# Optimization experiments

Hardware: AMD Instinct MI355X
Metric: run time of the kernel (lower is better)

## Reference

```python
import jax, jax.numpy as jnp
import numpy as np

E = 32      # num_embodiments
A = 64      # action_dim
H = 1024    # hidden_size
B = 64
T = 64


def setup_inputs() -> dict:
    key = jax.random.key(0)
    ks = jax.random.split(key, 9)
    return {
        "actions": jax.random.normal(ks[0], (B, T, A), dtype=jnp.float32),
        "W1_W": 0.02 * jax.random.normal(ks[1], (E, A, H), dtype=jnp.float32),
        "W1_b": jnp.zeros((E, H), dtype=jnp.float32),
        "W2_W": 0.02 * jax.random.normal(ks[2], (E, 2 * H, H), dtype=jnp.float32),
        "W2_b": jnp.zeros((E, H), dtype=jnp.float32),
        "W3_W": 0.02 * jax.random.normal(ks[3], (E, H, H), dtype=jnp.float32),
        "W3_b": jnp.zeros((E, H), dtype=jnp.float32),
        "timesteps": jax.random.randint(ks[4], (B,), 0, 1000, dtype=jnp.int32),
        "cat_ids": jax.random.randint(ks[5], (B,), 0, E, dtype=jnp.int32),
    }


def _cat_linear(x, W, b, cat_ids):
    # x: (B,T,in), W: (E,in,out), b: (E,out)
    Wg = W[cat_ids]               # (B,in,out) gathered per-batch weights
    bg = b[cat_ids]               # (B,out)
    return jnp.einsum('bti,bio->bto', x, Wg) + bg[:, None, :]


def _sinusoidal_pe(t, dim):
    # t: (B,T) float -> (B,T,dim)
    half = dim // 2
    exponent = -jnp.arange(half, dtype=jnp.float32) * (jnp.log(jnp.float32(10000.0)) / half)
    freqs = t[..., None] * jnp.exp(exponent)
    return jnp.concatenate([jnp.sin(freqs), jnp.cos(freqs)], axis=-1)


def reference(actions, W1_W, W1_b, W2_W, W2_b, W3_W, W3_b, timesteps, cat_ids):
    b, t, _ = actions.shape
    ts = jnp.broadcast_to(timesteps.astype(jnp.float32)[:, None], (b, t))  # (B,T)
    a_emb = _cat_linear(actions, W1_W, W1_b, cat_ids)                      # (B,T,H)
    tau_emb = _sinusoidal_pe(ts, H).astype(a_emb.dtype)                    # (B,T,H)
    x = jnp.concatenate([a_emb, tau_emb], axis=-1)                         # (B,T,2H)
    h = _cat_linear(x, W2_W, W2_b, cat_ids)
    x = h * jax.nn.sigmoid(h)                                              # swish
    return _cat_linear(x, W3_W, W3_b, cat_ids)                             # (B,T,H)
```

## Files before the change

### kernel.cpp

```cpp
#include <hip/hip_runtime.h>
#include <hip/hip_bf16.h>

#define NB 64
#define NT 64
#define NA 64
#define NH 1024
#define NE 32
#define K2DIM 2048

typedef unsigned short bf16_t;
typedef __attribute__((ext_vector_type(8))) short bf16x8;
typedef __attribute__((ext_vector_type(4))) short s16x4;
typedef __attribute__((ext_vector_type(4))) float f32x4;

__device__ __forceinline__ bf16_t f32_to_bf16(float f) {
    unsigned int u = __float_as_uint(f);
    u = (u + 0x7FFFu + ((u >> 16) & 1u)) >> 16;
    return (bf16_t)u;
}
__device__ __forceinline__ unsigned cvt2(float x, float y) {
    unsigned short a = __builtin_bit_cast(unsigned short, __float2bfloat16(x));
    unsigned short b = __builtin_bit_cast(unsigned short, __float2bfloat16(y));
    return (unsigned)a | ((unsigned)b << 16);
}

__global__ void make_groups(const int* __restrict__ cat_ids,
                            int* __restrict__ groups)
{
    __shared__ int keys[NB], order[NB], catv[NB];
    __shared__ int gcat[NB], gnb[NB], gb[NB][4];
    __shared__ int sng;

    const int tid = threadIdx.x;
    int c = cat_ids[tid];
    catv[tid] = c;
    keys[tid] = c * 64 + tid;
    __syncthreads();

    int mykey = keys[tid];
    int rank = 0;
    for (int j = 0; j < NB; ++j) rank += (keys[j] < mykey) ? 1 : 0;
    order[rank] = tid;
    __syncthreads();

    if (tid == 0) {
        int ng = 0, prev = -1, cnt = 4;
        for (int i = 0; i < NB; ++i) {
            int b  = order[i];
            int cb = catv[b];
            if (cb != prev || cnt == 4) {
                gcat[ng] = cb; gnb[ng] = 0; cnt = 0; prev = cb; ++ng;
            }
            gb[ng - 1][cnt] = b;
            ++cnt; gnb[ng - 1] = cnt;
        }
        sng = ng;
    }
    __syncthreads();

    int ng = sng;
    int base = tid * 8;
    if (tid < ng) {
        int nbv = gnb[tid];
        groups[base + 0] = gcat[tid];
        groups[base + 1] = nbv;
        #pragma unroll
        for (int s = 0; s < 4; ++s)
            groups[base + 2 + s] = gb[tid][s < nbv ? s : 0];
        groups[base + 6] = 0; groups[base + 7] = 0;
    } else {
        #pragma unroll
        for (int s = 0; s < 8; ++s) groups[base + s] = 0;
    }
}

__global__ __launch_bounds__(256) void k1_embed(
    const float* __restrict__ actions, const float* __restrict__ W1,
    const float* __restrict__ b1, const int* __restrict__ timesteps,
    const int* __restrict__ cat_ids, bf16_t* __restrict__ x)
{
    __shared__ float act[NT][NA];
    __shared__ float pe[64];

    const int b   = blockIdx.x;
    const int c0  = blockIdx.y * 64;
    const int tid = threadIdx.x;
    const int cat = cat_ids[b];
    const float ts = (float)timesteps[b];

    const float* ab = actions + b * (NT * NA);
    #pragma unroll
    for (int p = 0; p < 16; ++p) {
        int idx = tid + p * 256;
        act[idx >> 6][idx & 63] = ab[idx];
    }
    if (tid < 64) {
        const float kfreq = logf(10000.0f) / 512.0f;
        int c = c0 + tid;
        float v;
        if (c < 512) v = sinf(ts * expf(-(float)c * kfreq));
        else         v = cosf(ts * expf(-(float)(c - 512) * kfreq));
        pe[tid] = v;
    }
    __syncthreads();

    const int cc = tid & 63;
    const int c  = c0 + cc;
    const int t0 = tid >> 6;

    float acc[16];
    const float bias = b1[cat * NH + c];
    #pragma unroll
    for (int i = 0; i < 16; ++i) acc[i] = bias;

    const float* Wp = W1 + (size_t)cat * (NA * NH) + c;
    #pragma unroll 8
    for (int k = 0; k < NA; ++k) {
        float w = Wp[(size_t)k * NH];
        #pragma unroll
        for (int i = 0; i < 16; ++i)
            acc[i] = fmaf(act[t0 + 4 * i][k], w, acc[i]);
    }

    bf16_t* xb = x + (size_t)b * (NT * K2DIM);
    const bf16_t pv = f32_to_bf16(pe[cc]);
    #pragma unroll
    for (int i = 0; i < 16; ++i) {
        int t = t0 + 4 * i;
        xb[(size_t)t * K2DIM + c]      = f32_to_bf16(acc[i]);
        xb[(size_t)t * K2DIM + NH + c] = pv;
    }
}

template<int KDIM, bool SWISH, typename OutT>
__global__ __launch_bounds__(512) void gemm_grouped(
    const bf16_t* __restrict__ xin, const float* __restrict__ W,
    const float* __restrict__ bias, const int* __restrict__ groups,
    OutT* __restrict__ out)
{
    __shared__ __align__(128) char xs[4 * 8192];
    __shared__ __align__(128) char wsm[16384];

    const int* grp = groups + blockIdx.x * 8;
    const int nb = grp[1];
    if (nb == 0) return;
    const int cat = grp[0];
    int bslot[4];
    #pragma unroll
    for (int s = 0; s < 4; ++s) bslot[s] = grp[2 + s];

    const int n0   = blockIdx.y * 128;
    const int tid  = threadIdx.x;
    const int lane = tid & 63;
    const int wv   = tid >> 6;
    const int l15  = lane & 15;
    const int l4   = lane >> 4;
    const int msl  = wv & 3;
    const int pw   = (wv >> 2) * 4;
    const int ncol0 = n0 + (wv >> 2) * 64;

    constexpr int NK = KDIM / 64;

    const int xt  = tid >> 3;
    const int xk8 = tid & 7;
    const int xoff = ((xt * 128 + xk8 * 16) ^ ((xt & 7) << 4));
    const bf16_t* xsrc[4];
    #pragma unroll
    for (int p = 0; p < 4; ++p)
        xsrc[p] = xin + ((size_t)bslot[p] * NT + xt) * KDIM + xk8 * 8;
    const int wk  = tid >> 4;
    const int oct = tid & 15;
    const float* Wt0 = W + (size_t)cat * KDIM * NH + n0
                         + (size_t)wk * NH + oct * 8;
    int woff[2];
    #pragma unroll
    for (int p = 0; p < 2; ++p) {
        int kk = wk + 32 * p;
        woff[p] = ((kk >> 2) * 8 + (oct >> 1)) * 128 + (kk & 3) * 32 + (oct & 1) * 16;
    }

    f32x4 acc[4][4];
    #pragma unroll
    for (int nf = 0; nf < 4; ++nf) {
        float bv = bias[(size_t)cat * NH + ncol0 + nf * 16 + l15];
        #pragma unroll
        for (int mf = 0; mf < 4; ++mf)
            acc[mf][nf] = (f32x4){bv, bv, bv, bv};
    }

    const unsigned wbase = (unsigned)(unsigned long long)&wsm[0];
    const unsigned laneB = wbase + (unsigned)(l4 * 2048 + l15 * 8);
    const int aslot = msl * 8192;

    uint4  xr[4];
    float4 wr[4];

    auto LOAD = [&](int kc) {
        #pragma unroll
        for (int p = 0; p < 4; ++p)
            xr[p] = *(const uint4*)(xsrc[p] + (size_t)kc * 64);
        #pragma unroll
        for (int p = 0; p < 2; ++p) {
            const float* s = Wt0 + (size_t)(kc * 64 + 32 * p) * NH;
            wr[2 * p]     = *(const float4*)(s);
            wr[2 * p + 1] = *(const float4*)(s + 4);
        }
    };
    auto WRITE = [&]() {
        #pragma unroll
        for (int p = 0; p < 4; ++p)
            *(uint4*)(xs + xoff + p * 8192) = xr[p];
        #pragma unroll
        for (int p = 0; p < 2; ++p) {
            uint4 pk;
            pk.x = cvt2(wr[2 * p].x,     wr[2 * p].y);
            pk.y = cvt2(wr[2 * p].z,     wr[2 * p].w);
            pk.z = cvt2(wr[2 * p + 1].x, wr[2 * p + 1].y);
            pk.w = cvt2(wr[2 * p + 1].z, wr[2 * p + 1].w);
            *(uint4*)(wsm + woff[p]) = pk;
        }
    };

    LOAD(0);
    for (int kc = 0; kc < NK; ++kc) {
        __syncthreads();
        WRITE();
        __syncthreads();
        if (kc + 1 < NK) LOAD(kc + 1);

        #pragma unroll
        for (int ks = 0; ks < 2; ++ks) {
            bf16x8 af[4], bfr[4];
            #pragma unroll
            for (int mf = 0; mf < 4; ++mf) {
                int row = mf * 16 + l15;
                int off = aslot + ((row * 128 + ks * 64 + l4 * 16) ^ ((row & 7) << 4));
                af[mf] = *(const bf16x8*)(xs + off);
            }
            #pragma unroll
            for (int nf = 0; nf < 4; ++nf) {
                unsigned a = laneB + (unsigned)(ks * 8192 + (pw + nf) * 128);
                s16x4 lo, hi;
                asm volatile("ds_read_b64_tr_b16 %0, %1" : "=v"(lo) : "v"(a));
                asm volatile("ds_read_b64_tr_b16 %0, %1 offset:1024" : "=v"(hi) : "v"(a));
                bfr[nf] = __builtin_shufflevector(lo, hi, 0, 1, 2, 3, 4, 5, 6, 7);
            }
            asm volatile("s_waitcnt lgkmcnt(0)" ::: "memory");
            __builtin_amdgcn_sched_barrier(0);
            #pragma unroll
            for (int mf = 0; mf < 4; ++mf)
                #pragma unroll
                for (int nf = 0; nf < 4; ++nf)
                    acc[mf][nf] = __builtin_amdgcn_mfma_f32_16x16x32_bf16(
                        af[mf], bfr[nf], acc[mf][nf], 0, 0, 0);
        }
    }

    const int bout = bslot[msl];
    #pragma unroll
    for (int mf = 0; mf < 4; ++mf) {
        #pragma unroll
        for (int nf = 0; nf < 4; ++nf) {
            int col = ncol0 + nf * 16 + l15;
            #pragma unroll
            for (int r = 0; r < 4; ++r) {
                int trow = mf * 16 + l4 * 4 + r;
                float h = acc[mf][nf][r];
                if (SWISH) h = h / (1.0f + __expf(-h));
                if constexpr (sizeof(OutT) == 2) {
                    out[((size_t)bout * NT + trow) * NH + col] = (OutT)f32_to_bf16(h);
                } else {
                    out[((size_t)bout * NT + trow) * NH + col] = h;
                }
            }
        }
    }
}

extern "C" void kernel_launch(void* const* d_in, const int* in_sizes, int n_in,
                              void* d_out, int out_size, void* d_ws, size_t ws_size,
                              hipStream_t stream) {
    const float* actions   = (const float*)d_in[0];
    const float* W1        = (const float*)d_in[1];
    const float* b1        = (const float*)d_in[2];
    const float* W2        = (const float*)d_in[3];
    const float* b2        = (const float*)d_in[4];
    const float* W3        = (const float*)d_in[5];
    const float* b3        = (const float*)d_in[6];
    const int*   timesteps = (const int*)d_in[7];
    const int*   cat_ids   = (const int*)d_in[8];
    float* out = (float*)d_out;

    bf16_t* x = (bf16_t*)d_ws;
    bf16_t* y = x + (size_t)NB * NT * K2DIM;
    int* groups = (int*)(y + (size_t)NB * NT * NH);

    make_groups<<<1, 64, 0, stream>>>(cat_ids, groups);
    k1_embed<<<dim3(NB, NH / 64), 256, 0, stream>>>(actions, W1, b1, timesteps, cat_ids, x);
    gemm_grouped<K2DIM, true,  bf16_t><<<dim3(64, NH / 128), 512, 0, stream>>>(x, W2, b2, groups, y);
    gemm_grouped<NH,    false, float ><<<dim3(64, NH / 128), 512, 0, stream>>>(y, W3, b3, groups, out);
}
```

Baseline: 193.9 us.

## Shrink grouped GEMM tiles to two batches and double-buffer LDS

Batches now share an embodiment group in pairs rather than fours, and each block computes a 128x64 output tile with a 32-wide K chunk instead of 256x128 with 64-wide chunks. LDS is double-buffered, so there is one barrier per chunk and the next chunk's global load overlaps the MFMAs. The grid grows to 16x64 blocks with launch bounds allowing 4 blocks per CU, which raises occupancy and parallelism. The cost is more reloads of each weight tile, since fewer batches share it, and only four MFMAs per barrier, so the arithmetic per sync is small.

```diff
diff --git a/kernel.cpp b/kernel.cpp
--- a/kernel.cpp
+++ b/kernel.cpp
@@ -28,7 +28,7 @@
                             int* __restrict__ groups)
 {
     __shared__ int keys[NB], order[NB], catv[NB];
-    __shared__ int gcat[NB], gnb[NB], gb[NB][4];
+    __shared__ int gcat[NB], gnb[NB], gb[NB][2];
     __shared__ int sng;
 
     const int tid = threadIdx.x;
@@ -44,11 +44,11 @@
     __syncthreads();
 
     if (tid == 0) {
-        int ng = 0, prev = -1, cnt = 4;
+        int ng = 0, prev = -1, cnt = 2;
         for (int i = 0; i < NB; ++i) {
             int b  = order[i];
             int cb = catv[b];
-            if (cb != prev || cnt == 4) {
+            if (cb != prev || cnt == 2) {
                 gcat[ng] = cb; gnb[ng] = 0; cnt = 0; prev = cb; ++ng;
             }
             gb[ng - 1][cnt] = b;
@@ -64,9 +64,9 @@
         int nbv = gnb[tid];
         groups[base + 0] = gcat[tid];
         groups[base + 1] = nbv;
-        #pragma unroll
-        for (int s = 0; s < 4; ++s)
-            groups[base + 2 + s] = gb[tid][s < nbv ? s : 0];
+        groups[base + 2] = gb[tid][0];
+        groups[base + 3] = (nbv > 1) ? gb[tid][1] : gb[tid][0];
+        groups[base + 4] = 0; groups[base + 5] = 0;
         groups[base + 6] = 0; groups[base + 7] = 0;
     } else {
         #pragma unroll
@@ -133,139 +133,107 @@
 }
 
 template<int KDIM, bool SWISH, typename OutT>
-__global__ __launch_bounds__(512) void gemm_grouped(
+__global__ __launch_bounds__(512, 4) void gemm_g2(
     const bf16_t* __restrict__ xin, const float* __restrict__ W,
     const float* __restrict__ bias, const int* __restrict__ groups,
     OutT* __restrict__ out)
 {
-    __shared__ __align__(128) char xs[4 * 8192];
-    __shared__ __align__(128) char wsm[16384];
-
-    const int* grp = groups + blockIdx.x * 8;
+    __shared__ __align__(128) char lds[2][12288];
+
+    const int* grp = groups + blockIdx.y * 8;
     const int nb = grp[1];
     if (nb == 0) return;
     const int cat = grp[0];
-    int bslot[4];
-    #pragma unroll
-    for (int s = 0; s < 4; ++s) bslot[s] = grp[2 + s];
-
-    const int n0   = blockIdx.y * 128;
+    const int ba = grp[2];
+    const int bb = grp[3];
+
+    const int n0   = blockIdx.x * 64;
     const int tid  = threadIdx.x;
     const int lane = tid & 63;
     const int wv   = tid >> 6;
     const int l15  = lane & 15;
     const int l4   = lane >> 4;
-    const int msl  = wv & 3;
-    const int pw   = (wv >> 2) * 4;
-    const int ncol0 = n0 + (wv >> 2) * 64;
-
-    constexpr int NK = KDIM / 64;
-
-    const int xt  = tid >> 3;
-    const int xk8 = tid & 7;
-    const int xoff = ((xt * 128 + xk8 * 16) ^ ((xt & 7) << 4));
-    const bf16_t* xsrc[4];
-    #pragma unroll
-    for (int p = 0; p < 4; ++p)
-        xsrc[p] = xin + ((size_t)bslot[p] * NT + xt) * KDIM + xk8 * 8;
+    const int slot = wv >> 2;
+    const int nf   = wv & 3;
+
+    constexpr int NCH = KDIM / 32;
+
+    const int xs_s = tid >> 8;
+    const int xid  = tid & 255;
+    const int xt   = xid >> 2;
+    const int xoct = xid & 3;
+    const bf16_t* xg = xin + ((size_t)(xs_s ? bb : ba) * NT + xt) * KDIM + xoct * 8;
+    const int xl = xs_s * 4096 + xoct * 1024 + xt * 16;
+
     const int wk  = tid >> 4;
-    const int oct = tid & 15;
-    const float* Wt0 = W + (size_t)cat * KDIM * NH + n0
-                         + (size_t)wk * NH + oct * 8;
-    int woff[2];
-    #pragma unroll
-    for (int p = 0; p < 2; ++p) {
-        int kk = wk + 32 * p;
-        woff[p] = ((kk >> 2) * 8 + (oct >> 1)) * 128 + (kk & 3) * 32 + (oct & 1) * 16;
-    }
-
-    f32x4 acc[4][4];
-    #pragma unroll
-    for (int nf = 0; nf < 4; ++nf) {
-        float bv = bias[(size_t)cat * NH + ncol0 + nf * 16 + l15];
-        #pragma unroll
-        for (int mf = 0; mf < 4; ++mf)
-            acc[mf][nf] = (f32x4){bv, bv, bv, bv};
-    }
-
-    const unsigned wbase = (unsigned)(unsigned long long)&wsm[0];
-    const unsigned laneB = wbase + (unsigned)(l4 * 2048 + l15 * 8);
-    const int aslot = msl * 8192;
-
-    uint4  xr[4];
-    float4 wr[4];
-
+    const int wq4 = tid & 15;
+    const float* wg = W + (size_t)cat * KDIM * NH + (size_t)wk * NH + n0 + wq4 * 4;
+    const int wl = 8192 + ((wk >> 2) * 4 + (wq4 >> 2)) * 128
+                        + (wk & 3) * 32 + (wq4 & 3) * 8;
+
+    f32x4 acc[4];
+    {
+        float bv = bias[(size_t)cat * NH + n0 + nf * 16 + l15];
+        #pragma unroll
+        for (int mf = 0; mf < 4; ++mf) acc[mf] = (f32x4){bv, bv, bv, bv};
+    }
+
+    const unsigned ldsbase = (unsigned)(unsigned long long)&lds[0][0];
+    const unsigned trb = ldsbase + 8192u + (unsigned)(l4 * 1024 + nf * 128 + l15 * 8);
+    const int aoff = slot * 4096 + l4 * 1024 + l15 * 16;
+
+    uint4  xr;
+    float4 wr;
     auto LOAD = [&](int kc) {
-        #pragma unroll
-        for (int p = 0; p < 4; ++p)
-            xr[p] = *(const uint4*)(xsrc[p] + (size_t)kc * 64);
-        #pragma unroll
-        for (int p = 0; p < 2; ++p) {
-            const float* s = Wt0 + (size_t)(kc * 64 + 32 * p) * NH;
-            wr[2 * p]     = *(const float4*)(s);
-            wr[2 * p + 1] = *(const float4*)(s + 4);
-        }
+        xr = *(const uint4*)(xg + (size_t)kc * 32);
+        wr = *(const float4*)(wg + (size_t)kc * 32 * NH);
     };
-    auto WRITE = [&]() {
-        #pragma unroll
-        for (int p = 0; p < 4; ++p)
-            *(uint4*)(xs + xoff + p * 8192) = xr[p];
-        #pragma unroll
-        for (int p = 0; p < 2; ++p) {
-            uint4 pk;
-            pk.x = cvt2(wr[2 * p].x,     wr[2 * p].y);
-            pk.y = cvt2(wr[2 * p].z,     wr[2 * p].w);
-            pk.z = cvt2(wr[2 * p + 1].x, wr[2 * p + 1].y);
-            pk.w = cvt2(wr[2 * p + 1].z, wr[2 * p + 1].w);
-            *(uint4*)(wsm + woff[p]) = pk;
-        }
+    auto WRITE = [&](int pw) {
+        *(uint4*)(&lds[pw][0] + xl) = xr;
+        uint2 pk;
+        pk.x = cvt2(wr.x, wr.y);
+        pk.y = cvt2(wr.z, wr.w);
+        *(uint2*)(&lds[pw][0] + wl) = pk;
     };
 
     LOAD(0);
-    for (int kc = 0; kc < NK; ++kc) {
+    WRITE(0);
+    LOAD(1);
+
+    for (int kc = 0; kc < NCH; ++kc) {
+        const int p = kc & 1;
         __syncthreads();
-        WRITE();
-        __syncthreads();
-        if (kc + 1 < NK) LOAD(kc + 1);
-
-        #pragma unroll
-        for (int ks = 0; ks < 2; ++ks) {
-            bf16x8 af[4], bfr[4];
-            #pragma unroll
-            for (int mf = 0; mf < 4; ++mf) {
-                int row = mf * 16 + l15;
-                int off = aslot + ((row * 128 + ks * 64 + l4 * 16) ^ ((row & 7) << 4));
-                af[mf] = *(const bf16x8*)(xs + off);
-            }
-            #pragma unroll
-            for (int nf = 0; nf < 4; ++nf) {
-                unsigned a = laneB + (unsigned)(ks * 8192 + (pw + nf) * 128);
-                s16x4 lo, hi;
-                asm volatile("ds_read_b64_tr_b16 %0, %1" : "=v"(lo) : "v"(a));
-                asm volatile("ds_read_b64_tr_b16 %0, %1 offset:1024" : "=v"(hi) : "v"(a));
-                bfr[nf] = __builtin_shufflevector(lo, hi, 0, 1, 2, 3, 4, 5, 6, 7);
-            }
-            asm volatile("s_waitcnt lgkmcnt(0)" ::: "memory");
-            __builtin_amdgcn_sched_barrier(0);
-            #pragma unroll
-            for (int mf = 0; mf < 4; ++mf)
-                #pragma unroll
-                for (int nf = 0; nf < 4; ++nf)
-                    acc[mf][nf] = __builtin_amdgcn_mfma_f32_16x16x32_bf16(
-                        af[mf], bfr[nf], acc[mf][nf], 0, 0, 0);
-        }
-    }
-
-    const int bout = bslot[msl];
-    #pragma unroll
-    for (int mf = 0; mf < 4; ++mf) {
-        #pragma unroll
-        for (int nf = 0; nf < 4; ++nf) {
-            int col = ncol0 + nf * 16 + l15;
+
+        bf16x8 af0 = *(const bf16x8*)(&lds[p][0] + aoff);
+        bf16x8 af1 = *(const bf16x8*)(&lds[p][0] + aoff + 256);
+        bf16x8 af2 = *(const bf16x8*)(&lds[p][0] + aoff + 512);
+        bf16x8 af3 = *(const bf16x8*)(&lds[p][0] + aoff + 768);
+        unsigned a = trb + (unsigned)(p * 12288);
+        s16x4 lo, hi;
+        asm volatile("ds_read_b64_tr_b16 %0, %1" : "=v"(lo) : "v"(a));
+        asm volatile("ds_read_b64_tr_b16 %0, %1 offset:512" : "=v"(hi) : "v"(a));
+        bf16x8 bfr = __builtin_shufflevector(lo, hi, 0, 1, 2, 3, 4, 5, 6, 7);
+
+        asm volatile("s_waitcnt lgkmcnt(0)" ::: "memory");
+        __builtin_amdgcn_sched_barrier(0);
+        acc[0] = __builtin_amdgcn_mfma_f32_16x16x32_bf16(af0, bfr, acc[0], 0, 0, 0);
+        acc[1] = __builtin_amdgcn_mfma_f32_16x16x32_bf16(af1, bfr, acc[1], 0, 0, 0);
+        acc[2] = __builtin_amdgcn_mfma_f32_16x16x32_bf16(af2, bfr, acc[2], 0, 0, 0);
+        acc[3] = __builtin_amdgcn_mfma_f32_16x16x32_bf16(af3, bfr, acc[3], 0, 0, 0);
+
+        if (kc + 1 < NCH) WRITE(p ^ 1);
+        if (kc + 2 < NCH) LOAD(kc + 2);
+    }
+
+    if (slot < nb) {
+        const int bout = slot ? bb : ba;
+        const int col  = n0 + nf * 16 + l15;
+        #pragma unroll
+        for (int mf = 0; mf < 4; ++mf) {
             #pragma unroll
             for (int r = 0; r < 4; ++r) {
                 int trow = mf * 16 + l4 * 4 + r;
-                float h = acc[mf][nf][r];
+                float h = acc[mf][r];
                 if (SWISH) h = h / (1.0f + __expf(-h));
                 if constexpr (sizeof(OutT) == 2) {
                     out[((size_t)bout * NT + trow) * NH + col] = (OutT)f32_to_bf16(h);
@@ -297,6 +265,6 @@
 
     make_groups<<<1, 64, 0, stream>>>(cat_ids, groups);
     k1_embed<<<dim3(NB, NH / 64), 256, 0, stream>>>(actions, W1, b1, timesteps, cat_ids, x);
-    gemm_grouped<K2DIM, true,  bf16_t><<<dim3(64, NH / 128), 512, 0, stream>>>(x, W2, b2, groups, y);
-    gemm_grouped<NH,    false, float ><<<dim3(64, NH / 128), 512, 0, stream>>>(y, W3, b3, groups, out);
-}
+    gemm_g2<K2DIM, true,  bf16_t><<<dim3(16, 64), 512, 0, stream>>>(x, W2, b2, groups, y);
+    gemm_g2<NH,    false, float ><<<dim3(16, 64), 512, 0, stream>>>(y, W3, b3, groups, out);
+}
```

Result: faster. 176.7 us (-8.9%).
